# Optimization experiments

Hardware: AMD Instinct MI355X
Metric: run time of the kernel (lower is better)

The kernel has to match this reference:

```python
import jax, jax.numpy as jnp
import numpy as np

B = 65536
N_SPARSE = 26
N_DENSE = 13
EMB = 5
VOCAB = 100000
N_EXPERTS = 4
D_IN = N_DENSE + N_SPARSE * EMB  # 143
H1, H2 = 128, 64


def setup_inputs() -> dict:
    key = jax.random.key(0)
    ks = jax.random.split(key, 16)
    s = 0.05
    return {
        "sparse_inputs": jax.random.randint(ks[0], (B, N_SPARSE), 0, VOCAB),
        "dense_inputs": jax.random.normal(ks[1], (B, N_DENSE), dtype=jnp.float32),
        "emb_tables": jax.random.normal(ks[2], (N_SPARSE, VOCAB, EMB), dtype=jnp.float32) * s,
        "expert_W1": jax.random.normal(ks[3], (N_EXPERTS, D_IN, H1), dtype=jnp.float32) * s,
        "expert_b1": jnp.zeros((N_EXPERTS, H1), dtype=jnp.float32),
        "expert_W2": jax.random.normal(ks[4], (N_EXPERTS, H1, H2), dtype=jnp.float32) * s,
        "expert_b2": jnp.zeros((N_EXPERTS, H2), dtype=jnp.float32),
        "gate_finish_W": jax.random.normal(ks[5], (D_IN, N_EXPERTS), dtype=jnp.float32) * s,
        "gate_finish_b": jnp.zeros((N_EXPERTS,), dtype=jnp.float32),
        "gate_like_W": jax.random.normal(ks[6], (D_IN, N_EXPERTS), dtype=jnp.float32) * s,
        "gate_like_b": jnp.zeros((N_EXPERTS,), dtype=jnp.float32),
        "finish_W": jax.random.normal(ks[7], (H2, 1), dtype=jnp.float32) * s,
        "finish_b": jnp.zeros((1,), dtype=jnp.float32),
        "like_W": jax.random.normal(ks[8], (H2, 1), dtype=jnp.float32) * s,
        "like_b": jnp.zeros((1,), dtype=jnp.float32),
    }


def reference(sparse_inputs, dense_inputs, emb_tables, expert_W1, expert_b1,
              expert_W2, expert_b2, gate_finish_W, gate_finish_b,
              gate_like_W, gate_like_b, finish_W, finish_b, like_W, like_b):
    # per-feature embedding lookup: [B, N_SPARSE, EMB]
    feat_idx = jnp.arange(N_SPARSE)[None, :]
    sp_emb = emb_tables[feat_idx, sparse_inputs]
    x = jnp.concatenate([dense_inputs, sp_emb.reshape(sparse_inputs.shape[0], -1)], axis=1)  # [B, D_IN]

    # batched expert MLPs (dropout is inactive at inference)
    h = jax.nn.relu(jnp.einsum('bd,edh->beh', x, expert_W1) + expert_b1)  # [B, E, 128]
    expert_out = jax.nn.relu(jnp.einsum('beh,eho->beo', h, expert_W2) + expert_b2)  # [B, E, 64]

    gate_f = jax.nn.softmax(x @ gate_finish_W + gate_finish_b, axis=-1)  # [B, E]
    gate_l = jax.nn.softmax(x @ gate_like_W + gate_like_b, axis=-1)

    task_finish = jnp.einsum('be,beo->bo', gate_f, expert_out)  # [B, 64]
    task_like = jnp.einsum('be,beo->bo', gate_l, expert_out)

    finish = jax.nn.sigmoid(task_finish @ finish_W + finish_b)  # [B, 1]
    like = jax.nn.sigmoid(task_like @ like_W + like_b)  # [B, 1]
    return finish, like
```

## Files before the change

### kernel.cpp

```cpp
#include <hip/hip_runtime.h>
#include <math.h>

#define NB     65536
#define NSP    26
#define NDN    13
#define EMBD   5
#define VOCAB  100000
#define NE     4
#define DIN    143
#define KPAD   160
#define H1     128
#define H2     64

typedef __attribute__((ext_vector_type(8))) short bf16x8;
typedef __attribute__((ext_vector_type(4))) float f32x4;

__device__ __forceinline__ unsigned short f2bf(float f) {
    unsigned int u = __float_as_uint(f);
    u = (u + 0x7fff + ((u >> 16) & 1)) >> 16;
    return (unsigned short)u;
}

__device__ __forceinline__ unsigned cvtpk(float lo, float hi) {
    unsigned r;
    asm("v_cvt_pk_bf16_f32 %0, %1, %2" : "=v"(r) : "v"(lo), "v"(hi));
    return r;
}

__device__ __forceinline__ void gll16(const unsigned short* g, unsigned short* l) {
    __builtin_amdgcn_global_load_lds(
        (const __attribute__((address_space(1))) unsigned int*)g,
        (__attribute__((address_space(3))) unsigned int*)l, 16, 0, 0);
}

#define E1 (4*8*5*512)
#define E2 (4*4*4*512)
#define E3 (5*512)
#define NWE (E1+E2+E3)
#define GBLKS 1024
#define PBLKS ((NWE+255)/256)


__global__ __launch_bounds__(256)
void gather_pack(const int*   __restrict__ sparse,
                 const float* __restrict__ dense,
                 const float* __restrict__ emb,
                 const float* __restrict__ W1,  const float* __restrict__ W2,
                 const float* __restrict__ gfW, const float* __restrict__ glW,
                 unsigned short* __restrict__ w1p, unsigned short* __restrict__ w2p,
                 unsigned short* __restrict__ gwp, unsigned short* __restrict__ xg)
{
    const int blk = blockIdx.x;
    const int tid = threadIdx.x;
    if (blk < GBLKS) {
        __shared__ int idxs[64 * NSP];
        __shared__ __align__(16) unsigned short xs[64][168];
        const int row0 = blk * 64;

        for (int t = tid; t < 64 * NSP; t += 256)
            idxs[t] = sparse[row0 * NSP + t];
        for (int t = tid; t < 64 * NDN; t += 256) {
            int r = t / NDN, c = t - r * NDN;
            xs[r][c] = f2bf(dense[(row0 + r) * NDN + c]);
        }
        for (int t = tid; t < 64 * (KPAD - DIN); t += 256) {
            int r = t / (KPAD - DIN), c = DIN + (t - r * (KPAD - DIN));
            xs[r][c] = 0;
        }
        __syncthreads();
        for (int t = tid; t < 64 * NSP * EMBD; t += 256) {
            int f = t / (64 * EMBD);
            int rem = t - f * (64 * EMBD);
            int r = rem / EMBD, c = rem - r * EMBD;
            int idx = idxs[r * NSP + f];
            float v = emb[((size_t)f * VOCAB + idx) * EMBD + c];
            xs[r][NDN + f * EMBD + c] = f2bf(v);
        }
        __syncthreads();
        for (int v = tid; v < 4 * 5 * 64; v += 256) {
            int lo = v & 63, chunk = v >> 6;
            int s = chunk % 5, tl = chunk / 5;
            int b = lo & 15, g = lo >> 4;
            bf16x8 val = *(const bf16x8*)&xs[tl * 16 + b][32 * s + 8 * g];
            *(bf16x8*)(xg + ((size_t)((blk * 4 + tl) * 5 + s) * 64 + lo) * 8) = val;
        }
        return;
    }

    int i = (blk - GBLKS) * 256 + tid;
    if (i < E1) {
        int j = i & 7, l = (i >> 3) & 63;
        int rest = i >> 9;
        int s = rest % 5; rest /= 5;
        int nt = rest & 7, e = rest >> 3;
        int b = l & 15, g = l >> 4;
        int k = 32 * s + 8 * g + j;
        int n = nt * 16 + b;
        w1p[i] = (k < DIN) ? f2bf(W1[(e * DIN + k) * H1 + n]) : (unsigned short)0;
        return;
    }
    i -= E1;
    if (i < E2) {
        int j = i & 7, l = (i >> 3) & 63;
        int rest = i >> 9;
        int s = rest & 3; rest >>= 2;
        int ot = rest & 3, e = rest >> 2;
        int b = l & 15, g = l >> 4;
        int k = 32 * s + 8 * g + j;
        int o = ot * 16 + b;
        w2p[i] = f2bf(W2[(e * H1 + k) * H2 + o]);
        return;
    }
    i -= E2;
    if (i < E3) {
        int j = i & 7, l = (i >> 3) & 63;
        int s = i >> 9;
        int b = l & 15, g = l >> 4;
        int k = 32 * s + 8 * g + j;
        float v = 0.f;
        if (k < DIN) {
            if (b < 4)      v = gfW[k * NE + b];
            else if (b < 8) v = glW[k * NE + (b - 4)];
        }
        gwp[i] = f2bf(v);
    }
}

__global__ __launch_bounds__(256, 2)
void mmoe9(const unsigned short* __restrict__ xg,
           const unsigned short* __restrict__ w1p, const float* __restrict__ b1,
           const unsigned short* __restrict__ w2p, const float* __restrict__ b2,
           const unsigned short* __restrict__ gwp,
           const float* __restrict__ gfb, const float* __restrict__ glb,
           const float* __restrict__ fW,  const float* __restrict__ lW,
           float* __restrict__ acc)
{
    __shared__ __align__(16) unsigned short wlds[28672];
    __shared__ __align__(16) char hsb[16384];

    const int tid  = threadIdx.x;
    const int wid  = tid >> 6;
    const int lane = tid & 63;
    const int b    = lane & 15;
    const int g    = lane >> 4;
    const int rg   = blockIdx.x >> 2;
    const int e    = blockIdx.x & 3;
    const int t0   = rg * 8 + wid * 2;
    const int swz  = (b & 7) << 4;
    char* const hw = hsb + wid * 4096 + b * 128;

    #pragma unroll
    for (int i = 0; i < 14; ++i) {
        int c = wid * 14 + i;
        if (c < 40)
            gll16(w1p + (((size_t)e * 40 + c) * 64 + lane) * 8, wlds + c * 512);
        else
            gll16(w2p + (((size_t)e * 16 + (c - 40)) * 64 + lane) * 8,
                  wlds + 20480 + (c - 40) * 512);
    }

    bf16x8 xf[2][5];
    #pragma unroll
    for (int rt = 0; rt < 2; ++rt)
        #pragma unroll
        for (int s = 0; s < 5; ++s)
            xf[rt][s] = *(const bf16x8*)(xg + ((size_t)((t0 + rt) * 5 + s) * 64 + lane) * 8);

    f32x4 ga[2];
    ga[0] = (f32x4){0.f, 0.f, 0.f, 0.f};
    ga[1] = (f32x4){0.f, 0.f, 0.f, 0.f};
    #pragma unroll
    for (int s = 0; s < 5; ++s) {
        bf16x8 af = *(const bf16x8*)(gwp + (size_t)(s * 64 + lane) * 8);
        ga[0] = __builtin_amdgcn_mfma_f32_16x16x32_bf16(af, xf[0][s], ga[0], 0, 0, 0);
        ga[1] = __builtin_amdgcn_mfma_f32_16x16x32_bf16(af, xf[1][s], ga[1], 0, 0, 0);
    }
    const float4 gfb4 = *(const float4*)gfb;
    const float4 glb4 = *(const float4*)glb;
    float gfv[2], glv[2];
    #pragma unroll
    for (int rt = 0; rt < 2; ++rt) {
        const float4 bias = (g == 1) ? glb4 : gfb4;
        float l0 = ga[rt][0] + bias.x, l1 = ga[rt][1] + bias.y;
        float l2 = ga[rt][2] + bias.z, l3 = ga[rt][3] + bias.w;
        float m = fmaxf(fmaxf(l0, l1), fmaxf(l2, l3));
        float e0 = expf(l0 - m), e1 = expf(l1 - m), e2 = expf(l2 - m), e3 = expf(l3 - m);
        float inv = 1.f / (e0 + e1 + e2 + e3);
        float sel = (e == 0) ? e0 : (e == 1) ? e1 : (e == 2) ? e2 : e3;
        sel *= inv;
        gfv[rt] = __shfl(sel, b);
        glv[rt] = __shfl(sel, b + 16);
    }

    __syncthreads();

    float vf[2] = {0.f, 0.f}, vl[2] = {0.f, 0.f};
    f32x4 c[2][4];
    #pragma unroll
    for (int rt = 0; rt < 2; ++rt)
        #pragma unroll
        for (int ot = 0; ot < 4; ++ot)
            c[rt][ot] = (f32x4){0.f, 0.f, 0.f, 0.f};

    #pragma unroll
    for (int h = 0; h < 2; ++h) {
        #pragma unroll
        for (int nl = 0; nl < 4; ++nl) {
            const int nt = h * 4 + nl;
            bf16x8 wv[5];
            #pragma unroll
            for (int s = 0; s < 5; ++s)
                wv[s] = *(const bf16x8*)(wlds + ((nt * 5 + s) * 64 + lane) * 8);
            f32x4 a2[2];
            a2[0] = (f32x4){0.f, 0.f, 0.f, 0.f};
            a2[1] = (f32x4){0.f, 0.f, 0.f, 0.f};
            #pragma unroll
            for (int s = 0; s < 5; ++s) {
                a2[0] = __builtin_amdgcn_mfma_f32_16x16x32_bf16(wv[s], xf[0][s], a2[0], 0, 0, 0);
                a2[1] = __builtin_amdgcn_mfma_f32_16x16x32_bf16(wv[s], xf[1][s], a2[1], 0, 0, 0);
            }
            const float4 b1v = *(const float4*)(b1 + e * H1 + nt * 16 + 4 * g);
            #pragma unroll
            for (int rt = 0; rt < 2; ++rt) {
                uint2 hv;
                hv.x = cvtpk(fmaxf(a2[rt][0] + b1v.x, 0.f), fmaxf(a2[rt][1] + b1v.y, 0.f));
                hv.y = cvtpk(fmaxf(a2[rt][2] + b1v.z, 0.f), fmaxf(a2[rt][3] + b1v.w, 0.f));
                *(uint2*)(hw + rt * 2048 + ((nl * 32 + g * 8) ^ swz)) = hv;
            }
        }
        bf16x8 hf[2][2];
        #pragma unroll
        for (int sl = 0; sl < 2; ++sl)
            #pragma unroll
            for (int rt = 0; rt < 2; ++rt)
                hf[sl][rt] = *(const bf16x8*)(hw + rt * 2048 + ((sl * 64 + g * 16) ^ swz));
        #pragma unroll
        for (int ot = 0; ot < 4; ++ot) {
            #pragma unroll
            for (int sl = 0; sl < 2; ++sl) {
                bf16x8 wv2 = *(const bf16x8*)(wlds + 20480 + ((ot * 4 + h * 2 + sl) * 64 + lane) * 8);
                c[0][ot] = __builtin_amdgcn_mfma_f32_16x16x32_bf16(wv2, hf[sl][0], c[0][ot], 0, 0, 0);
                c[1][ot] = __builtin_amdgcn_mfma_f32_16x16x32_bf16(wv2, hf[sl][1], c[1][ot], 0, 0, 0);
            }
        }
    }

    #pragma unroll
    for (int ot = 0; ot < 4; ++ot) {
        const float4 b2v = *(const float4*)(b2 + e * H2 + ot * 16 + 4 * g);
        const float4 fwv = *(const float4*)(fW + ot * 16 + 4 * g);
        const float4 lwv = *(const float4*)(lW + ot * 16 + 4 * g);
        #pragma unroll
        for (int rt = 0; rt < 2; ++rt) {
            float o0 = fmaxf(c[rt][ot][0] + b2v.x, 0.f), o1 = fmaxf(c[rt][ot][1] + b2v.y, 0.f);
            float o2 = fmaxf(c[rt][ot][2] + b2v.z, 0.f), o3 = fmaxf(c[rt][ot][3] + b2v.w, 0.f);
            vf[rt] += gfv[rt] * (o0 * fwv.x + o1 * fwv.y + o2 * fwv.z + o3 * fwv.w);
            vl[rt] += glv[rt] * (o0 * lwv.x + o1 * lwv.y + o2 * lwv.z + o3 * lwv.w);
        }
    }

    #pragma unroll
    for (int rt = 0; rt < 2; ++rt) {
        float f = vf[rt], l = vl[rt];
        f += __shfl_xor(f, 16); f += __shfl_xor(f, 32);
        l += __shfl_xor(l, 16); l += __shfl_xor(l, 32);
        if (g == 0) {
            int r = (t0 + rt) * 16 + b;
            acc[(size_t)e * NB + r]            = f;
            acc[(size_t)(4 + e) * NB + r]      = l;
        }
    }
}

__global__ __launch_bounds__(256)
void heads_ep(const float* __restrict__ acc,
              const float* __restrict__ fb, const float* __restrict__ lb,
              float* __restrict__ out)
{
    int r = blockIdx.x * 256 + threadIdx.x;
    float sf = acc[r] + acc[NB + r] + acc[2 * NB + r] + acc[3 * NB + r];
    float sl = acc[4 * NB + r] + acc[5 * NB + r] + acc[6 * NB + r] + acc[7 * NB + r];
    out[r]      = 1.f / (1.f + expf(-(sf + fb[0])));
    out[NB + r] = 1.f / (1.f + expf(-(sl + lb[0])));
}


__global__ __launch_bounds__(256)
void preproc(const float* __restrict__ W1, const float* __restrict__ W2,
             const float* __restrict__ gfW, const float* __restrict__ glW,
             unsigned short* __restrict__ w1t, unsigned short* __restrict__ w2t,
             unsigned short* __restrict__ gwc)
{
    int i = blockIdx.x * 256 + threadIdx.x;
    if (i < 4*128*160) {
        int k = i % KPAD;
        int n = (i / KPAD) & (H1 - 1);
        int e = i / (KPAD * H1);
        w1t[i] = (k < DIN) ? f2bf(W1[(e * DIN + k) * H1 + n]) : (unsigned short)0;
    } else if (i < 4*128*160 + 4*64*128) {
        int j = i - 4*128*160;
        int k = j & (H1 - 1);
        int o = (j >> 7) & (H2 - 1);
        int e = j >> 13;
        w2t[j] = f2bf(W2[(e * H1 + k) * H2 + o]);
    } else if (i < 4*128*160 + 4*64*128 + 16*160) {
        int j = i - (4*128*160 + 4*64*128);
        int k = j % KPAD;
        int r = j / KPAD;
        float v = 0.f;
        if (k < DIN) {
            if (r < 4)      v = gfW[k * NE + r];
            else if (r < 8) v = glW[k * NE + (r - 4)];
        }
        gwc[j] = f2bf(v);
    }
}

__global__ __launch_bounds__(256)
void mmoe_mfma(const int*   __restrict__ sparse,
               const float* __restrict__ dense,
               const float* __restrict__ emb,
               const unsigned short* __restrict__ w1t,
               const float* __restrict__ b1,
               const unsigned short* __restrict__ w2t,
               const float* __restrict__ b2,
               const unsigned short* __restrict__ gwc,
               const float* __restrict__ gfb, const float* __restrict__ glb,
               const float* __restrict__ fW,  const float* __restrict__ fb,
               const float* __restrict__ lW,  const float* __restrict__ lb,
               float* __restrict__ out)
{
    __shared__ __align__(16) unsigned short xs[64][KPAD];
    __shared__ __align__(16) unsigned short hs[64][136];
    __shared__ __align__(16) float gts[64][8];

    const int tid   = threadIdx.x;
    const int wid   = tid >> 6;
    const int lane  = tid & 63;
    const int b     = lane & 15;
    const int g     = lane >> 4;
    const int rbase = wid * 16;
    const int grow0 = blockIdx.x * 64 + rbase;

    for (int t = lane; t < 16 * NDN; t += 64) {
        int r = t & 15, d = t >> 4;
        xs[rbase + r][d] = f2bf(dense[(grow0 + r) * NDN + d]);
    }
    for (int t = lane; t < 16 * (KPAD - DIN); t += 64) {
        int r = t & 15, d = DIN + (t >> 4);
        xs[rbase + r][d] = 0;
    }
    for (int t = lane; t < 16 * NSP; t += 64) {
        int r = t & 15, f = t >> 4;
        int idx = sparse[(grow0 + r) * NSP + f];
        const float* ep = emb + (f * VOCAB + idx) * EMBD;
        int c0 = NDN + EMBD * f;
        #pragma unroll
        for (int c = 0; c < EMBD; ++c)
            xs[rbase + r][c0 + c] = f2bf(ep[c]);
    }

    bf16x8 xf[5];
    #pragma unroll
    for (int s = 0; s < 5; ++s)
        xf[s] = *(const bf16x8*)&xs[rbase + b][32 * s + 8 * g];

    f32x4 ga = {0.f, 0.f, 0.f, 0.f};
    #pragma unroll
    for (int s = 0; s < 5; ++s) {
        bf16x8 af = *(const bf16x8*)(gwc + b * KPAD + 32 * s + 8 * g);
        ga = __builtin_amdgcn_mfma_f32_16x16x32_bf16(af, xf[s], ga, 0, 0, 0);
    }
    if (g < 2) {
        const float4 bias = *(const float4*)(g ? glb : gfb);
        float l0 = ga[0] + bias.x, l1 = ga[1] + bias.y;
        float l2 = ga[2] + bias.z, l3 = ga[3] + bias.w;
        float m = fmaxf(fmaxf(l0, l1), fmaxf(l2, l3));
        float e0 = expf(l0 - m), e1 = expf(l1 - m), e2 = expf(l2 - m), e3 = expf(l3 - m);
        float inv = 1.f / (e0 + e1 + e2 + e3);
        float4 gv; gv.x = e0 * inv; gv.y = e1 * inv; gv.z = e2 * inv; gv.w = e3 * inv;
        *(float4*)&gts[rbase + b][g * 4] = gv;
    }

    float vf = 0.f, vl = 0.f;
    for (int e = 0; e < NE; ++e) {
        const unsigned short* w1e = w1t + e * (H1 * KPAD);
        #pragma unroll
        for (int nt = 0; nt < 8; ++nt) {
            f32x4 acc = {0.f, 0.f, 0.f, 0.f};
            #pragma unroll
            for (int s = 0; s < 5; ++s) {
                bf16x8 af = *(const bf16x8*)(w1e + (nt * 16 + b) * KPAD + 32 * s + 8 * g);
                acc = __builtin_amdgcn_mfma_f32_16x16x32_bf16(af, xf[s], acc, 0, 0, 0);
            }
            const float4 b1v = *(const float4*)(b1 + e * H1 + nt * 16 + 4 * g);
            unsigned lo = (unsigned)f2bf(fmaxf(acc[0] + b1v.x, 0.f)) |
                          ((unsigned)f2bf(fmaxf(acc[1] + b1v.y, 0.f)) << 16);
            unsigned hi = (unsigned)f2bf(fmaxf(acc[2] + b1v.z, 0.f)) |
                          ((unsigned)f2bf(fmaxf(acc[3] + b1v.w, 0.f)) << 16);
            uint2 hv; hv.x = lo; hv.y = hi;
            *(uint2*)&hs[rbase + b][nt * 16 + 4 * g] = hv;
        }

        bf16x8 hf[4];
        #pragma unroll
        for (int s = 0; s < 4; ++s)
            hf[s] = *(const bf16x8*)&hs[rbase + b][32 * s + 8 * g];

        float gf = gts[rbase + b][e];
        float gl = gts[rbase + b][4 + e];
        const unsigned short* w2e = w2t + e * (H2 * H1);
        #pragma unroll
        for (int ot = 0; ot < 4; ++ot) {
            f32x4 acc = {0.f, 0.f, 0.f, 0.f};
            #pragma unroll
            for (int s = 0; s < 4; ++s) {
                bf16x8 af = *(const bf16x8*)(w2e + (ot * 16 + b) * H1 + 32 * s + 8 * g);
                acc = __builtin_amdgcn_mfma_f32_16x16x32_bf16(af, hf[s], acc, 0, 0, 0);
            }
            const float4 b2v = *(const float4*)(b2 + e * H2 + ot * 16 + 4 * g);
            const float4 fwv = *(const float4*)(fW + ot * 16 + 4 * g);
            const float4 lwv = *(const float4*)(lW + ot * 16 + 4 * g);
            float o0 = fmaxf(acc[0] + b2v.x, 0.f);
            float o1 = fmaxf(acc[1] + b2v.y, 0.f);
            float o2 = fmaxf(acc[2] + b2v.z, 0.f);
            float o3 = fmaxf(acc[3] + b2v.w, 0.f);
            vf += gf * (o0 * fwv.x + o1 * fwv.y + o2 * fwv.z + o3 * fwv.w);
            vl += gl * (o0 * lwv.x + o1 * lwv.y + o2 * lwv.z + o3 * lwv.w);
        }
    }

    vf += __shfl_xor(vf, 16); vf += __shfl_xor(vf, 32);
    vl += __shfl_xor(vl, 16); vl += __shfl_xor(vl, 32);
    if (g == 0) {
        int r = grow0 + b;
        out[r]      = 1.f / (1.f + expf(-(vf + fb[0])));
        out[NB + r] = 1.f / (1.f + expf(-(vl + lb[0])));
    }
}


extern "C" void kernel_launch(void* const* d_in, const int* in_sizes, int n_in,
                              void* d_out, int out_size, void* d_ws, size_t ws_size,
                              hipStream_t stream) {
    const int*   sparse = (const int*)  d_in[0];
    const float* dense  = (const float*)d_in[1];
    const float* emb    = (const float*)d_in[2];
    const float* W1     = (const float*)d_in[3];
    const float* b1     = (const float*)d_in[4];
    const float* W2     = (const float*)d_in[5];
    const float* b2     = (const float*)d_in[6];
    const float* gfW    = (const float*)d_in[7];
    const float* gfb    = (const float*)d_in[8];
    const float* glW    = (const float*)d_in[9];
    const float* glb    = (const float*)d_in[10];
    const float* fW     = (const float*)d_in[11];
    const float* fb     = (const float*)d_in[12];
    const float* lW     = (const float*)d_in[13];
    const float* lb     = (const float*)d_in[14];

    const size_t XG_BYTES  = (size_t)NB * KPAD * 2;
    const size_t W_BYTES   = (size_t)NWE * 2;
    const size_t ACC_BYTES = (size_t)2 * 4 * NB * 4;
    const size_t NEED = XG_BYTES + W_BYTES + ACC_BYTES;

    if (ws_size >= NEED) {
        unsigned short* xg  = (unsigned short*)d_ws;
        unsigned short* w1p = (unsigned short*)((char*)d_ws + XG_BYTES);
        unsigned short* w2p = (unsigned short*)((char*)d_ws + XG_BYTES + (size_t)E1 * 2);
        unsigned short* gwp = (unsigned short*)((char*)d_ws + XG_BYTES + (size_t)(E1 + E2) * 2);
        float*          acc = (float*)((char*)d_ws + XG_BYTES + W_BYTES);

        gather_pack<<<GBLKS + PBLKS, 256, 0, stream>>>(
            sparse, dense, emb, W1, W2, gfW, glW, w1p, w2p, gwp, xg);
        mmoe9<<<(NB / 128) * 4, 256, 0, stream>>>(xg, w1p, b1, w2p, b2, gwp,
                                                  gfb, glb, fW, lW, acc);
        heads_ep<<<NB / 256, 256, 0, stream>>>(acc, fb, lb, (float*)d_out);
    } else {
        unsigned short* w1t = (unsigned short*)d_ws;
        unsigned short* w2t = (unsigned short*)((char*)d_ws + 163840);
        unsigned short* gwc = (unsigned short*)((char*)d_ws + 229376);

        int tot = 4*128*160 + 4*64*128 + 16*160;
        preproc<<<(tot + 255) / 256, 256, 0, stream>>>(W1, W2, gfW, glW, w1t, w2t, gwc);
        mmoe_mfma<<<NB / 64, 256, 0, stream>>>(sparse, dense, emb,
                                               w1t, b1, w2t, b2, gwc,
                                               gfb, glb, fW, fb, lW, lb,
                                               (float*)d_out);
    }
}
```

Before: 68.57 us.

## Use 512-thread blocks with one row tile per wave and remapped block order

The expert MLP kernel now runs 8 waves per block, each handling a single 16-row tile instead of two. The launch bound rises to 512 threads with 4 blocks per CU, and the grid becomes 2048 blocks. Block indices are remapped so the four experts of a row group sit in nearby blocks, which should improve L2 reuse of the packed activations. This halves per-wave registers and raises occupancy, but each wave gets less MFMA reuse of the weight fragments it loads from LDS.

```diff
diff --git a/kernel.cpp b/kernel.cpp
--- a/kernel.cpp
+++ b/kernel.cpp
@@ -126,14 +126,14 @@
     }
 }
 
-__global__ __launch_bounds__(256, 2)
-void mmoe9(const unsigned short* __restrict__ xg,
-           const unsigned short* __restrict__ w1p, const float* __restrict__ b1,
-           const unsigned short* __restrict__ w2p, const float* __restrict__ b2,
-           const unsigned short* __restrict__ gwp,
-           const float* __restrict__ gfb, const float* __restrict__ glb,
-           const float* __restrict__ fW,  const float* __restrict__ lW,
-           float* __restrict__ acc)
+__global__ __launch_bounds__(512, 4)
+void mmoe10(const unsigned short* __restrict__ xg,
+            const unsigned short* __restrict__ w1p, const float* __restrict__ b1,
+            const unsigned short* __restrict__ w2p, const float* __restrict__ b2,
+            const unsigned short* __restrict__ gwp,
+            const float* __restrict__ gfb, const float* __restrict__ glb,
+            const float* __restrict__ fW,  const float* __restrict__ lW,
+            float* __restrict__ acc)
 {
     __shared__ __align__(16) unsigned short wlds[28672];
     __shared__ __align__(16) char hsb[16384];
@@ -143,15 +143,17 @@
     const int lane = tid & 63;
     const int b    = lane & 15;
     const int g    = lane >> 4;
-    const int rg   = blockIdx.x >> 2;
-    const int e    = blockIdx.x & 3;
-    const int t0   = rg * 8 + wid * 2;
+    const int q    = blockIdx.x >> 5;
+    const int r5   = blockIdx.x & 31;
+    const int e    = r5 >> 3;
+    const int rg   = q * 8 + (r5 & 7);
+    const int t0   = rg * 8 + wid;
     const int swz  = (b & 7) << 4;
-    char* const hw = hsb + wid * 4096 + b * 128;
-
-    #pragma unroll
-    for (int i = 0; i < 14; ++i) {
-        int c = wid * 14 + i;
+    char* const hw = hsb + wid * 2048 + b * 128;
+
+    #pragma unroll
+    for (int i = 0; i < 7; ++i) {
+        int c = wid * 7 + i;
         if (c < 40)
             gll16(w1p + (((size_t)e * 40 + c) * 64 + lane) * 8, wlds + c * 512);
         else
@@ -159,48 +161,38 @@
                   wlds + 20480 + (c - 40) * 512);
     }
 
-    bf16x8 xf[2][5];
-    #pragma unroll
-    for (int rt = 0; rt < 2; ++rt)
-        #pragma unroll
-        for (int s = 0; s < 5; ++s)
-            xf[rt][s] = *(const bf16x8*)(xg + ((size_t)((t0 + rt) * 5 + s) * 64 + lane) * 8);
-
-    f32x4 ga[2];
-    ga[0] = (f32x4){0.f, 0.f, 0.f, 0.f};
-    ga[1] = (f32x4){0.f, 0.f, 0.f, 0.f};
+    bf16x8 xf[5];
+    #pragma unroll
+    for (int s = 0; s < 5; ++s)
+        xf[s] = *(const bf16x8*)(xg + ((size_t)(t0 * 5 + s) * 64 + lane) * 8);
+
+    f32x4 ga = {0.f, 0.f, 0.f, 0.f};
     #pragma unroll
     for (int s = 0; s < 5; ++s) {
         bf16x8 af = *(const bf16x8*)(gwp + (size_t)(s * 64 + lane) * 8);
-        ga[0] = __builtin_amdgcn_mfma_f32_16x16x32_bf16(af, xf[0][s], ga[0], 0, 0, 0);
-        ga[1] = __builtin_amdgcn_mfma_f32_16x16x32_bf16(af, xf[1][s], ga[1], 0, 0, 0);
+        ga = __builtin_amdgcn_mfma_f32_16x16x32_bf16(af, xf[s], ga, 0, 0, 0);
     }
     const float4 gfb4 = *(const float4*)gfb;
     const float4 glb4 = *(const float4*)glb;
-    float gfv[2], glv[2];
-    #pragma unroll
-    for (int rt = 0; rt < 2; ++rt) {
+    float gfv, glv;
+    {
         const float4 bias = (g == 1) ? glb4 : gfb4;
-        float l0 = ga[rt][0] + bias.x, l1 = ga[rt][1] + bias.y;
-        float l2 = ga[rt][2] + bias.z, l3 = ga[rt][3] + bias.w;
+        float l0 = ga[0] + bias.x, l1 = ga[1] + bias.y;
+        float l2 = ga[2] + bias.z, l3 = ga[3] + bias.w;
         float m = fmaxf(fmaxf(l0, l1), fmaxf(l2, l3));
         float e0 = expf(l0 - m), e1 = expf(l1 - m), e2 = expf(l2 - m), e3 = expf(l3 - m);
         float inv = 1.f / (e0 + e1 + e2 + e3);
         float sel = (e == 0) ? e0 : (e == 1) ? e1 : (e == 2) ? e2 : e3;
         sel *= inv;
-        gfv[rt] = __shfl(sel, b);
-        glv[rt] = __shfl(sel, b + 16);
+        gfv = __shfl(sel, b);
+        glv = __shfl(sel, b + 16);
     }
 
     __syncthreads();
 
-    float vf[2] = {0.f, 0.f}, vl[2] = {0.f, 0.f};
-    f32x4 c[2][4];
-    #pragma unroll
-    for (int rt = 0; rt < 2; ++rt)
-        #pragma unroll
-        for (int ot = 0; ot < 4; ++ot)
-            c[rt][ot] = (f32x4){0.f, 0.f, 0.f, 0.f};
+    f32x4 c[4];
+    #pragma unroll
+    for (int ot = 0; ot < 4; ++ot) c[ot] = (f32x4){0.f, 0.f, 0.f, 0.f};
 
     #pragma unroll
     for (int h = 0; h < 2; ++h) {
@@ -211,64 +203,48 @@
             #pragma unroll
             for (int s = 0; s < 5; ++s)
                 wv[s] = *(const bf16x8*)(wlds + ((nt * 5 + s) * 64 + lane) * 8);
-            f32x4 a2[2];
-            a2[0] = (f32x4){0.f, 0.f, 0.f, 0.f};
-            a2[1] = (f32x4){0.f, 0.f, 0.f, 0.f};
+            f32x4 a2 = {0.f, 0.f, 0.f, 0.f};
             #pragma unroll
-            for (int s = 0; s < 5; ++s) {
-                a2[0] = __builtin_amdgcn_mfma_f32_16x16x32_bf16(wv[s], xf[0][s], a2[0], 0, 0, 0);
-                a2[1] = __builtin_amdgcn_mfma_f32_16x16x32_bf16(wv[s], xf[1][s], a2[1], 0, 0, 0);
-            }
+            for (int s = 0; s < 5; ++s)
+                a2 = __builtin_amdgcn_mfma_f32_16x16x32_bf16(wv[s], xf[s], a2, 0, 0, 0);
             const float4 b1v = *(const float4*)(b1 + e * H1 + nt * 16 + 4 * g);
-            #pragma unroll
-            for (int rt = 0; rt < 2; ++rt) {
-                uint2 hv;
-                hv.x = cvtpk(fmaxf(a2[rt][0] + b1v.x, 0.f), fmaxf(a2[rt][1] + b1v.y, 0.f));
-                hv.y = cvtpk(fmaxf(a2[rt][2] + b1v.z, 0.f), fmaxf(a2[rt][3] + b1v.w, 0.f));
-                *(uint2*)(hw + rt * 2048 + ((nl * 32 + g * 8) ^ swz)) = hv;
-            }
-        }
-        bf16x8 hf[2][2];
+            uint2 hv;
+            hv.x = cvtpk(fmaxf(a2[0] + b1v.x, 0.f), fmaxf(a2[1] + b1v.y, 0.f));
+            hv.y = cvtpk(fmaxf(a2[2] + b1v.z, 0.f), fmaxf(a2[3] + b1v.w, 0.f));
+            *(uint2*)(hw + ((nl * 32 + g * 8) ^ swz)) = hv;
+        }
+        bf16x8 hf[2];
         #pragma unroll
         for (int sl = 0; sl < 2; ++sl)
-            #pragma unroll
-            for (int rt = 0; rt < 2; ++rt)
-                hf[sl][rt] = *(const bf16x8*)(hw + rt * 2048 + ((sl * 64 + g * 16) ^ swz));
+            hf[sl] = *(const bf16x8*)(hw + ((sl * 64 + g * 16) ^ swz));
         #pragma unroll
         for (int ot = 0; ot < 4; ++ot) {
             #pragma unroll
             for (int sl = 0; sl < 2; ++sl) {
-                bf16x8 wv2 = *(const bf16x8*)(wlds + 20480 + ((ot * 4 + h * 2 + sl) * 64 + lane) * 8);
-                c[0][ot] = __builtin_amdgcn_mfma_f32_16x16x32_bf16(wv2, hf[sl][0], c[0][ot], 0, 0, 0);
-                c[1][ot] = __builtin_amdgcn_mfma_f32_16x16x32_bf16(wv2, hf[sl][1], c[1][ot], 0, 0, 0);
+                bf16x8 wv2 = *(const bf16x8*)(wlds + 20480 + ((ot * 4 + 2 * h + sl) * 64 + lane) * 8);
+                c[ot] = __builtin_amdgcn_mfma_f32_16x16x32_bf16(wv2, hf[sl], c[ot], 0, 0, 0);
             }
         }
     }
 
+    float vf = 0.f, vl = 0.f;
     #pragma unroll
     for (int ot = 0; ot < 4; ++ot) {
         const float4 b2v = *(const float4*)(b2 + e * H2 + ot * 16 + 4 * g);
         const float4 fwv = *(const float4*)(fW + ot * 16 + 4 * g);
         const float4 lwv = *(const float4*)(lW + ot * 16 + 4 * g);
-        #pragma unroll
-        for (int rt = 0; rt < 2; ++rt) {
-            float o0 = fmaxf(c[rt][ot][0] + b2v.x, 0.f), o1 = fmaxf(c[rt][ot][1] + b2v.y, 0.f);
-            float o2 = fmaxf(c[rt][ot][2] + b2v.z, 0.f), o3 = fmaxf(c[rt][ot][3] + b2v.w, 0.f);
-            vf[rt] += gfv[rt] * (o0 * fwv.x + o1 * fwv.y + o2 * fwv.z + o3 * fwv.w);
-            vl[rt] += glv[rt] * (o0 * lwv.x + o1 * lwv.y + o2 * lwv.z + o3 * lwv.w);
-        }
-    }
-
-    #pragma unroll
-    for (int rt = 0; rt < 2; ++rt) {
-        float f = vf[rt], l = vl[rt];
-        f += __shfl_xor(f, 16); f += __shfl_xor(f, 32);
-        l += __shfl_xor(l, 16); l += __shfl_xor(l, 32);
-        if (g == 0) {
-            int r = (t0 + rt) * 16 + b;
-            acc[(size_t)e * NB + r]            = f;
-            acc[(size_t)(4 + e) * NB + r]      = l;
-        }
+        float o0 = fmaxf(c[ot][0] + b2v.x, 0.f), o1 = fmaxf(c[ot][1] + b2v.y, 0.f);
+        float o2 = fmaxf(c[ot][2] + b2v.z, 0.f), o3 = fmaxf(c[ot][3] + b2v.w, 0.f);
+        vf += gfv * (o0 * fwv.x + o1 * fwv.y + o2 * fwv.z + o3 * fwv.w);
+        vl += glv * (o0 * lwv.x + o1 * lwv.y + o2 * lwv.z + o3 * lwv.w);
+    }
+
+    vf += __shfl_xor(vf, 16); vf += __shfl_xor(vf, 32);
+    vl += __shfl_xor(vl, 16); vl += __shfl_xor(vl, 32);
+    if (g == 0) {
+        int r = t0 * 16 + b;
+        acc[(size_t)e * NB + r]       = vf;
+        acc[(size_t)(4 + e) * NB + r] = vl;
     }
 }
 
@@ -473,8 +449,8 @@
 
         gather_pack<<<GBLKS + PBLKS, 256, 0, stream>>>(
             sparse, dense, emb, W1, W2, gfW, glW, w1p, w2p, gwp, xg);
-        mmoe9<<<(NB / 128) * 4, 256, 0, stream>>>(xg, w1p, b1, w2p, b2, gwp,
-                                                  gfb, glb, fW, lW, acc);
+        mmoe10<<<2048, 512, 0, stream>>>(xg, w1p, b1, w2p, b2, gwp,
+                                         gfb, glb, fW, lW, acc);
         heads_ep<<<NB / 256, 256, 0, stream>>>(acc, fb, lb, (float*)d_out);
     } else {
         unsigned short* w1t = (unsigned short*)d_ws;
```

After: 63.45 us. 7.5% less time.
